# Kernel tuning notes

Measured on AMD Instinct MI355X. Metric: run time of the kernel, lower is better.

Reference implementation:

```python
import jax, jax.numpy as jnp
import numpy as np

CURV_BOUNDS = (-2.0, 2.0)
THRESH = 0.01   # |k| below this -> Euclidean branch
EPS = 1e-5

B, S, D = 4, 2048, 512


def setup_inputs() -> dict:
    key = jax.random.key(0)
    ks = jax.random.split(key, 8)
    x = jax.random.normal(ks[0], (B, S, D), jnp.float32)
    sc = 1.0 / np.sqrt(D)  # ~ nn.Linear default init scale
    Wq = jax.random.uniform(ks[1], (D, D), jnp.float32, -sc, sc)
    bq = jax.random.uniform(ks[2], (D,), jnp.float32, -sc, sc)
    Wk = jax.random.uniform(ks[3], (D, D), jnp.float32, -sc, sc)
    bk = jax.random.uniform(ks[4], (D,), jnp.float32, -sc, sc)
    Wv = jax.random.uniform(ks[5], (D, D), jnp.float32, -sc, sc)
    bv = jax.random.uniform(ks[6], (D,), jnp.float32, -sc, sc)
    curvature_raw = jnp.float32(0.5)   # init_curvature
    temperature = jnp.float32(1.0)
    mask = jnp.triu(jnp.ones((S, S), dtype=bool), 1)  # causal: True = masked out
    return {"x": x, "Wq": Wq, "bq": bq, "Wk": Wk, "bk": bk, "Wv": Wv,
            "bv": bv, "curvature_raw": curvature_raw,
            "temperature": temperature, "mask": mask}


def _curvature(raw):
    k_min, k_max = CURV_BOUNDS
    return k_min + (k_max - k_min) * (jnp.tanh(raw) + 1.0) / 2.0


def _project(u, k):
    # project_to_manifold: identity (euclid), Poincare-ball clip (k<0), sphere renorm (k>0)
    n = jnp.sqrt(jnp.sum(u * u, axis=-1, keepdims=True) + 1e-12)
    absk = jnp.abs(k)
    sk = jnp.sqrt(jnp.maximum(absk, EPS))
    max_norm = (1.0 - 1e-3) / sk                      # ball radius 1/sqrt(|k|)
    u_hyp = u * jnp.minimum(1.0, max_norm / n)
    u_sph = u / (n * sk)                              # sphere radius 1/sqrt(k)
    return jnp.where(absk < THRESH, u, jnp.where(k < 0, u_hyp, u_sph))


def reference(x, Wq, bq, Wk, bk, Wv, bv, curvature_raw, temperature, mask):
    k = _curvature(curvature_raw)
    q = x @ Wq.T + bq
    kk = x @ Wk.T + bk
    v = x @ Wv.T + bv
    qm = _project(q, k)
    km = _project(kk, k)

    # pairwise quantities without materializing [B,S,S,D]
    dots = jnp.einsum('bid,bjd->bij', qm, km)         # [B,S,S]
    qn2 = jnp.sum(qm * qm, axis=-1)                   # [B,S]
    kn2 = jnp.sum(km * km, axis=-1)                   # [B,S]
    diff2 = jnp.maximum(qn2[:, :, None] + kn2[:, None, :] - 2.0 * dots, 0.0)

    absk = jnp.abs(k)
    sk = jnp.sqrt(jnp.maximum(absk, EPS))

    d_euc = jnp.sqrt(diff2 + 1e-12)
    # hyperbolic (Poincare ball, c=|k|): acosh(1 + 2c|x-y|^2 / ((1-c|x|^2)(1-c|y|^2))) / sqrt(c)
    denom = jnp.maximum((1.0 - absk * qn2)[:, :, None] * (1.0 - absk * kn2)[:, None, :], EPS)
    arg = 1.0 + 2.0 * absk * diff2 / denom
    d_hyp = jnp.arccosh(jnp.maximum(arg, 1.0 + 1e-7)) / sk
    # spherical (radius 1/sqrt(k)): arccos(k * <x,y>) / sqrt(k)
    cosang = jnp.clip(absk * dots, -1.0 + 1e-7, 1.0 - 1e-7)
    d_sph = jnp.arccos(cosang) / sk

    dist = jnp.where(absk < THRESH, d_euc, jnp.where(k < 0, d_hyp, d_sph))

    scores = -dist / (temperature + 1e-8)
    scores = jnp.where(mask[None, :, :], -jnp.inf, scores)
    attention = jax.nn.softmax(scores, axis=-1)       # [B,S,S]
    output = jnp.einsum('bij,bjd->bid', attention, v) # [B,S,D]
    return output, attention
```

## Files before the change

### kernel.cpp

```cpp
#include <hip/hip_runtime.h>
#include <hip/hip_bf16.h>
#include <math.h>

typedef unsigned short u16;
typedef float float4e __attribute__((ext_vector_type(4)));
typedef short short8 __attribute__((ext_vector_type(8)));
typedef unsigned short ushort8 __attribute__((ext_vector_type(8)));
typedef unsigned short u16x4 __attribute__((ext_vector_type(4)));

#define SEQ 2048
#define DIM 512
#define NB  4

__device__ __forceinline__ float bf2f(u16 h) {
    return __uint_as_float(((unsigned)h) << 16);
}
__device__ __forceinline__ u16 f2bf(float f) {
    __hip_bfloat16 h = __float2bfloat16(f);
    return *reinterpret_cast<u16*>(&h);
}
__device__ __forceinline__ float curv_of(float raw) {
    return -2.0f + 2.0f * (tanhf(raw) + 1.0f);
}
__device__ __forceinline__ float fast_acos(float x) {
    float ax = fabsf(x);
    float r = sqrtf(fmaxf(1.f - ax, 0.f)) *
              (1.5707288f + ax * (-0.2121144f + ax * (0.0742610f - 0.0187293f * ax)));
    return (x < 0.f) ? (3.14159265f - r) : r;
}
__device__ __forceinline__ void gl_lds16(const u16* g, u16* lds) {
    __builtin_amdgcn_global_load_lds(
        (const __attribute__((address_space(1))) unsigned int*)g,
        (__attribute__((address_space(3))) unsigned int*)lds, 16, 0, 0);
}

__global__ __launch_bounds__(256, 8) void qkv_kernel(
    const float* __restrict__ xf,
    const float* __restrict__ Wq, const float* __restrict__ Wk, const float* __restrict__ Wv,
    const float* __restrict__ bq, const float* __restrict__ bk, const float* __restrict__ bv,
    u16* __restrict__ qk, u16* __restrict__ vT)
{
    int bn = blockIdx.x, bm = blockIdx.y;

    __shared__ __align__(16) u16 As[64 * 64];
    __shared__ __align__(16) u16 Bs[64 * 64];

    int t = threadIdx.x, wave = t >> 6, lane = t & 63;
    int wr = wave >> 1, wc = wave & 1;
    int lrow = lane & 15, quad = lane >> 4;
    int srow = lane >> 3, sc = lane & 7;

    const float* Af = xf + (size_t)(bm * 64) * 512;
    const float* Wsel = (bn < 8) ? Wq : (bn < 16 ? Wk : Wv);
    const float* Bf = Wsel + (size_t)((bn & 7) * 64) * 512;

    float4e acc[2][2];
#pragma unroll
    for (int i = 0; i < 2; i++)
#pragma unroll
        for (int j = 0; j < 2; j++) acc[i][j] = (float4e){0.f, 0.f, 0.f, 0.f};

    for (int kt = 0; kt < 8; ++kt) {
        int k0 = kt << 6;
        __syncthreads();
#pragma unroll
        for (int h = 0; h < 2; ++h) {
            int q = wave * 2 + h;
            int row = q * 8 + srow;
            int c = sc ^ srow;
            const float* ga = Af + (size_t)row * 512 + k0 + c * 8;
            float4 a0 = *(const float4*)ga, a1 = *(const float4*)(ga + 4);
            const float* gb = Bf + (size_t)row * 512 + k0 + c * 8;
            float4 b0 = *(const float4*)gb, b1 = *(const float4*)(gb + 4);
            ushort8 ha, hb;
            ha[0] = f2bf(a0.x); ha[1] = f2bf(a0.y); ha[2] = f2bf(a0.z); ha[3] = f2bf(a0.w);
            ha[4] = f2bf(a1.x); ha[5] = f2bf(a1.y); ha[6] = f2bf(a1.z); ha[7] = f2bf(a1.w);
            hb[0] = f2bf(b0.x); hb[1] = f2bf(b0.y); hb[2] = f2bf(b0.z); hb[3] = f2bf(b0.w);
            hb[4] = f2bf(b1.x); hb[5] = f2bf(b1.y); hb[6] = f2bf(b1.z); hb[7] = f2bf(b1.w);
            *(ushort8*)&As[(size_t)row * 64 + sc * 8] = ha;
            *(ushort8*)&Bs[(size_t)row * 64 + sc * 8] = hb;
        }
        __syncthreads();
#pragma unroll
        for (int s = 0; s < 2; ++s) {
            short8 af[2], bfr[2];
#pragma unroll
            for (int im = 0; im < 2; im++) {
                int R = wr * 32 + im * 16 + lrow;
                af[im] = *(const short8*)&As[R * 64 + (((s * 4 + quad) ^ (R & 7)) * 8)];
            }
#pragma unroll
            for (int in = 0; in < 2; in++) {
                int R = wc * 32 + in * 16 + lrow;
                bfr[in] = *(const short8*)&Bs[R * 64 + (((s * 4 + quad) ^ (R & 7)) * 8)];
            }
#pragma unroll
            for (int im = 0; im < 2; im++)
#pragma unroll
                for (int in = 0; in < 2; in++)
                    acc[im][in] = __builtin_amdgcn_mfma_f32_16x16x32_bf16(af[im], bfr[in], acc[im][in], 0, 0, 0);
        }
    }

#pragma unroll
    for (int im = 0; im < 2; im++)
#pragma unroll
        for (int in = 0; in < 2; in++) {
            int gi0 = bm * 64 + wr * 32 + im * 16 + quad * 4;
            int gj = bn * 64 + wc * 32 + in * 16 + lrow;
            float bias = (gj < 512) ? bq[gj] : (gj < 1024 ? bk[gj - 512] : bv[gj - 1024]);
            if (gj < 1024) {
#pragma unroll
                for (int r = 0; r < 4; r++)
                    qk[(size_t)(gi0 + r) * 1024 + gj] = f2bf(acc[im][in][r] + bias);
            } else {
                u16x4 pack;
#pragma unroll
                for (int r = 0; r < 4; r++) pack[r] = f2bf(acc[im][in][r] + bias);
                int bb = gi0 >> 11, s = gi0 & 2047;
                *(u16x4*)&vT[((size_t)bb * DIM + (gj - 1024)) * SEQ + s] = pack;
            }
        }
}

template<int MODE>
__global__ __launch_bounds__(256, 8) void gemm64_kernel(
    const u16* __restrict__ A, int lda, long long sA,
    const u16* __restrict__ Bt, int ldb, long long sB,
    void* __restrict__ Cv, int ldc, long long sC,
    float* __restrict__ lsum,
    const float* __restrict__ qn2v, const float* __restrict__ kn2v,
    const float* __restrict__ sclqv, const float* __restrict__ sclkv,
    const float* __restrict__ curvp, const float* __restrict__ tempp)
{
    int bn = blockIdx.x, b = blockIdx.z;
    int bm = (MODE == 2) ? (gridDim.y - 1 - blockIdx.y) : blockIdx.y;
    if (MODE == 1 && bn > bm) return;

    __shared__ __align__(16) u16 As[64 * 64];
    __shared__ __align__(16) u16 Bs[64 * 64];

    int t = threadIdx.x, wave = t >> 6, lane = t & 63;
    int wr = wave >> 1, wc = wave & 1;
    int lrow = lane & 15, quad = lane >> 4;
    int srow = lane >> 3, sc = lane & 7;

    const u16* Ab = A + (size_t)b * sA + (size_t)(bm * 64) * lda;
    const u16* Bb = Bt + (size_t)b * sB + (size_t)(bn * 64) * ldb;

    float4e acc[2][2];
#pragma unroll
    for (int i = 0; i < 2; i++)
#pragma unroll
        for (int j = 0; j < 2; j++) acc[i][j] = (float4e){0.f, 0.f, 0.f, 0.f};

    int kIters = (MODE == 2) ? (bm + 1) : 8;

    for (int kt = 0; kt < kIters; ++kt) {
        int k0 = kt << 6;
        __syncthreads();
#pragma unroll
        for (int h = 0; h < 2; ++h) {
            int q = wave * 2 + h;
            int row = q * 8 + srow;
            int c = sc ^ srow;
            gl_lds16(Ab + (size_t)row * lda + k0 + c * 8, &As[q * 512]);
            gl_lds16(Bb + (size_t)row * ldb + k0 + c * 8, &Bs[q * 512]);
        }
        __syncthreads();
#pragma unroll
        for (int s = 0; s < 2; ++s) {
            short8 af[2], bfr[2];
#pragma unroll
            for (int im = 0; im < 2; im++) {
                int R = wr * 32 + im * 16 + lrow;
                af[im] = *(const short8*)&As[R * 64 + (((s * 4 + quad) ^ (R & 7)) * 8)];
            }
#pragma unroll
            for (int in = 0; in < 2; in++) {
                int R = wc * 32 + in * 16 + lrow;
                bfr[in] = *(const short8*)&Bs[R * 64 + (((s * 4 + quad) ^ (R & 7)) * 8)];
            }
#pragma unroll
            for (int im = 0; im < 2; im++)
#pragma unroll
                for (int in = 0; in < 2; in++)
                    acc[im][in] = __builtin_amdgcn_mfma_f32_16x16x32_bf16(af[im], bfr[in], acc[im][in], 0, 0, 0);
        }
    }

    if (MODE == 1) {
        float kv = curv_of(curvp[0]);
        float absk = fabsf(kv);
        float sk = sqrtf(fmaxf(absk, 1e-5f));
        float invsk = 1.0f / sk;
        float invT = 1.0f / (tempp[0] + 1e-8f);
        u16* Cb = (u16*)Cv + (size_t)b * sC;

        float psum[2][4];
#pragma unroll
        for (int im = 0; im < 2; im++)
#pragma unroll
            for (int r = 0; r < 4; r++) psum[im][r] = 0.f;

#pragma unroll
        for (int im = 0; im < 2; im++) {
#pragma unroll
            for (int r = 0; r < 4; r++) {
                int gi = bm * 64 + wr * 32 + im * 16 + quad * 4 + r;
                float qn = qn2v[b * SEQ + gi];
                float sq = sclqv[b * SEQ + gi];
#pragma unroll
                for (int in = 0; in < 2; in++) {
                    int gj = bn * 64 + wc * 32 + in * 16 + lrow;
                    float kn = kn2v[b * SEQ + gj];
                    float dot = acc[im][in][r] * sq * sclkv[b * SEQ + gj];
                    float diff2 = fmaxf(qn + kn - 2.f * dot, 0.f);
                    float dist;
                    if (absk < 0.01f) {
                        dist = sqrtf(diff2 + 1e-12f);
                    } else if (kv < 0.f) {
                        float denom = fmaxf((1.f - absk * qn) * (1.f - absk * kn), 1e-5f);
                        float arg = fmaxf(1.f + 2.f * absk * diff2 / denom, 1.f + 1e-7f);
                        dist = acoshf(arg) * invsk;
                    } else {
                        float c = fminf(fmaxf(absk * dot, -1.f + 1e-7f), 1.f - 1e-7f);
                        dist = fast_acos(c) * invsk;
                    }
                    float s = -dist * invT;
                    float e = (gj <= gi) ? __expf(s) : 0.f;
                    Cb[(size_t)gi * ldc + gj] = f2bf(e);
                    psum[im][r] += e;
                }
            }
        }
#pragma unroll
        for (int im = 0; im < 2; im++)
#pragma unroll
            for (int r = 0; r < 4; r++) {
                float v = psum[im][r];
                v += __shfl_xor(v, 1);
                v += __shfl_xor(v, 2);
                v += __shfl_xor(v, 4);
                v += __shfl_xor(v, 8);
                if (lrow == 0) {
                    int gi = bm * 64 + wr * 32 + im * 16 + quad * 4 + r;
                    atomicAdd(&lsum[b * SEQ + gi], v);
                }
            }
    } else {
        float* Cb = (float*)Cv + (size_t)b * sC;
#pragma unroll
        for (int im = 0; im < 2; im++)
#pragma unroll
            for (int r = 0; r < 4; r++) {
                int gi = bm * 64 + wr * 32 + im * 16 + quad * 4 + r;
                float invl = 1.0f / lsum[b * SEQ + gi];
#pragma unroll
                for (int in = 0; in < 2; in++) {
                    int gd = bn * 64 + wc * 32 + in * 16 + lrow;
                    Cb[(size_t)gi * ldc + gd] = acc[im][in][r] * invl;
                }
            }
    }
}

__global__ __launch_bounds__(256) void project_kernel(
    const u16* __restrict__ qk,
    float* __restrict__ qn2, float* __restrict__ kn2,
    float* __restrict__ sclqv, float* __restrict__ sclkv,
    float* __restrict__ lsum,
    const float* __restrict__ curvp)
{
    if (threadIdx.x < 4) lsum[blockIdx.x * 4 + threadIdx.x] = 0.f;

    int wave = threadIdx.x >> 6, lane = threadIdx.x & 63;
    int r = blockIdx.x * 4 + wave;
    float kv = curv_of(curvp[0]);
    float absk = fabsf(kv);
    float sk = sqrtf(fmaxf(absk, 1e-5f));

    const u16* row = qk + (size_t)r * 1024;
    ushort8 qh = *(const ushort8*)&row[lane * 8];
    ushort8 kh = *(const ushort8*)&row[512 + lane * 8];

    float sq = 0.f, s2 = 0.f;
#pragma unroll
    for (int e = 0; e < 8; e++) {
        float qv = bf2f(qh[e]); sq += qv * qv;
        float kw = bf2f(kh[e]); s2 += kw * kw;
    }
#pragma unroll
    for (int off = 1; off < 64; off <<= 1) {
        sq += __shfl_xor(sq, off);
        s2 += __shfl_xor(s2, off);
    }

    if (lane == 0) {
        float nq = sqrtf(sq + 1e-12f);
        float nk = sqrtf(s2 + 1e-12f);
        float sclq, sclk;
        if (absk < 0.01f) { sclq = 1.f; sclk = 1.f; }
        else if (kv < 0.f) {
            float mx = (1.0f - 1e-3f) / sk;
            sclq = fminf(1.f, mx / nq);
            sclk = fminf(1.f, mx / nk);
        } else {
            sclq = 1.f / (nq * sk);
            sclk = 1.f / (nk * sk);
        }
        qn2[r] = sq * sclq * sclq;
        kn2[r] = s2 * sclk * sclk;
        sclqv[r] = sclq;
        sclkv[r] = sclk;
    }
}

__global__ __launch_bounds__(256) void norm_attn_kernel(
    const u16* __restrict__ attnH, const float* __restrict__ lsum,
    float* __restrict__ attnF)
{
    int i = blockIdx.x, b = blockIdx.y, t = threadIdx.x;
    float inv = 1.0f / lsum[b * SEQ + i];
    const u16* rowh = attnH + ((size_t)b * SEQ + i) * SEQ;
    float* row = attnF + ((size_t)b * SEQ + i) * SEQ;
    int L = i + 1;
    int j0 = t * 8;
    float4 lo, hi;
    if (j0 + 8 <= L) {
        ushort8 h = *(const ushort8*)&rowh[j0];
        lo.x = bf2f(h[0]) * inv; lo.y = bf2f(h[1]) * inv;
        lo.z = bf2f(h[2]) * inv; lo.w = bf2f(h[3]) * inv;
        hi.x = bf2f(h[4]) * inv; hi.y = bf2f(h[5]) * inv;
        hi.z = bf2f(h[6]) * inv; hi.w = bf2f(h[7]) * inv;
    } else {
        float v[8];
#pragma unroll
        for (int e = 0; e < 8; e++)
            v[e] = (j0 + e < L) ? bf2f(rowh[j0 + e]) * inv : 0.f;
        lo = (float4){v[0], v[1], v[2], v[3]};
        hi = (float4){v[4], v[5], v[6], v[7]};
    }
    *(float4*)&row[j0] = lo;
    *(float4*)&row[j0 + 4] = hi;
}

extern "C" void kernel_launch(void* const* d_in, const int* in_sizes, int n_in,
                              void* d_out, int out_size, void* d_ws, size_t ws_size,
                              hipStream_t stream) {
    (void)in_sizes; (void)n_in; (void)out_size; (void)ws_size;

    const float* x    = (const float*)d_in[0];
    const float* Wq   = (const float*)d_in[1];
    const float* bq   = (const float*)d_in[2];
    const float* Wk   = (const float*)d_in[3];
    const float* bk   = (const float*)d_in[4];
    const float* Wv   = (const float*)d_in[5];
    const float* bv   = (const float*)d_in[6];
    const float* curv = (const float*)d_in[7];
    const float* temp = (const float*)d_in[8];

    float* out   = (float*)d_out;
    float* attnF = out + (size_t)NB * SEQ * DIM;

    char* ws = (char*)d_ws;
    u16*   attnH = (u16*)(ws + 0);
    u16*   qk    = (u16*)(ws + 33554432);
    u16*   vT    = (u16*)(ws + 50331648);
    float* qn2   = (float*)(ws + 58720256);
    float* kn2   = (float*)(ws + 58753024);
    float* sclq  = (float*)(ws + 58785792);
    float* sclk  = (float*)(ws + 58818560);
    float* lsum  = (float*)(ws + 58851328);

    qkv_kernel<<<dim3(1536 / 64, 8192 / 64, 1), 256, 0, stream>>>(
        x, Wq, Wk, Wv, bq, bk, bv, qk, vT);

    project_kernel<<<NB * SEQ / 4, 256, 0, stream>>>(qk, qn2, kn2, sclq, sclk, lsum, curv);

    gemm64_kernel<1><<<dim3(SEQ / 64, SEQ / 64, NB), 256, 0, stream>>>(
        qk, 1024, (long long)SEQ * 1024, qk + 512, 1024, (long long)SEQ * 1024,
        (void*)attnH, SEQ, (long long)SEQ * SEQ,
        lsum, qn2, kn2, sclq, sclk, curv, temp);

    gemm64_kernel<2><<<dim3(DIM / 64, SEQ / 64, NB), 256, 0, stream>>>(
        attnH, SEQ, (long long)SEQ * SEQ, vT, SEQ, (long long)DIM * SEQ,
        (void*)out, DIM, (long long)SEQ * DIM,
        lsum, nullptr, nullptr, nullptr, nullptr, nullptr, nullptr);

    norm_attn_kernel<<<dim3(SEQ, NB), 256, 0, stream>>>(attnH, lsum, attnF);
}
```

Measured before the change: 247.1 us.

## Merge PV GEMM and attention normalization into one launch; swizzle QKV block order

The PV GEMM and the attention-row normalization now run as two roles of one kernel. Blocks with x<8 do the PV product and the rest write the normalized fp32 attention tiles, so the bandwidth-bound normalize work overlaps the compute-bound, triangular-imbalanced GEMM instead of running after it. The QKV projection kernel also remaps block ids so groups of 8 row tiles sweep all column tiles together, which is meant to improve L2 reuse of the weights. The cost is that both roles share one launch config and LDS allocation, and the normalize role now uses 64-row tiles.

After: 247.5 us. Within noise of the previous version (+0.2%).

```diff
diff --git a/kernel.cpp b/kernel.cpp
--- a/kernel.cpp
+++ b/kernel.cpp
@@ -40,7 +40,12 @@
     const float* __restrict__ bq, const float* __restrict__ bk, const float* __restrict__ bv,
     u16* __restrict__ qk, u16* __restrict__ vT)
 {
-    int bn = blockIdx.x, bm = blockIdx.y;
+    int id = blockIdx.y * 24 + blockIdx.x;
+    int k8 = id & 7;
+    int rest = id >> 3;
+    int bn = rest % 24;
+    int g  = rest / 24;
+    int bm = g * 8 + k8;
 
     __shared__ __align__(16) u16 As[64 * 64];
     __shared__ __align__(16) u16 Bs[64 * 64];
@@ -123,19 +128,16 @@
         }
 }
 
-template<int MODE>
-__global__ __launch_bounds__(256, 8) void gemm64_kernel(
-    const u16* __restrict__ A, int lda, long long sA,
-    const u16* __restrict__ Bt, int ldb, long long sB,
-    void* __restrict__ Cv, int ldc, long long sC,
+__global__ __launch_bounds__(256, 8) void scores_kernel(
+    const u16* __restrict__ qk,
+    u16* __restrict__ attnH,
     float* __restrict__ lsum,
     const float* __restrict__ qn2v, const float* __restrict__ kn2v,
     const float* __restrict__ sclqv, const float* __restrict__ sclkv,
     const float* __restrict__ curvp, const float* __restrict__ tempp)
 {
-    int bn = blockIdx.x, b = blockIdx.z;
-    int bm = (MODE == 2) ? (gridDim.y - 1 - blockIdx.y) : blockIdx.y;
-    if (MODE == 1 && bn > bm) return;
+    int bn = blockIdx.x, bm = blockIdx.y, b = blockIdx.z;
+    if (bn > bm) return;
 
     __shared__ __align__(16) u16 As[64 * 64];
     __shared__ __align__(16) u16 Bs[64 * 64];
@@ -145,8 +147,8 @@
     int lrow = lane & 15, quad = lane >> 4;
     int srow = lane >> 3, sc = lane & 7;
 
-    const u16* Ab = A + (size_t)b * sA + (size_t)(bm * 64) * lda;
-    const u16* Bb = Bt + (size_t)b * sB + (size_t)(bn * 64) * ldb;
+    const u16* Ab = qk + (size_t)b * SEQ * 1024 + (size_t)(bm * 64) * 1024;
+    const u16* Bb = qk + 512 + (size_t)b * SEQ * 1024 + (size_t)(bn * 64) * 1024;
 
     float4e acc[2][2];
 #pragma unroll
@@ -154,9 +156,7 @@
 #pragma unroll
         for (int j = 0; j < 2; j++) acc[i][j] = (float4e){0.f, 0.f, 0.f, 0.f};
 
-    int kIters = (MODE == 2) ? (bm + 1) : 8;
-
-    for (int kt = 0; kt < kIters; ++kt) {
+    for (int kt = 0; kt < 8; ++kt) {
         int k0 = kt << 6;
         __syncthreads();
 #pragma unroll
@@ -164,8 +164,8 @@
             int q = wave * 2 + h;
             int row = q * 8 + srow;
             int c = sc ^ srow;
-            gl_lds16(Ab + (size_t)row * lda + k0 + c * 8, &As[q * 512]);
-            gl_lds16(Bb + (size_t)row * ldb + k0 + c * 8, &Bs[q * 512]);
+            gl_lds16(Ab + (size_t)row * 1024 + k0 + c * 8, &As[q * 512]);
+            gl_lds16(Bb + (size_t)row * 1024 + k0 + c * 8, &Bs[q * 512]);
         }
         __syncthreads();
 #pragma unroll
@@ -189,67 +189,129 @@
         }
     }
 
-    if (MODE == 1) {
-        float kv = curv_of(curvp[0]);
-        float absk = fabsf(kv);
-        float sk = sqrtf(fmaxf(absk, 1e-5f));
-        float invsk = 1.0f / sk;
-        float invT = 1.0f / (tempp[0] + 1e-8f);
-        u16* Cb = (u16*)Cv + (size_t)b * sC;
-
-        float psum[2][4];
-#pragma unroll
-        for (int im = 0; im < 2; im++)
-#pragma unroll
-            for (int r = 0; r < 4; r++) psum[im][r] = 0.f;
-
-#pragma unroll
-        for (int im = 0; im < 2; im++) {
-#pragma unroll
-            for (int r = 0; r < 4; r++) {
+    float kv = curv_of(curvp[0]);
+    float absk = fabsf(kv);
+    float sk = sqrtf(fmaxf(absk, 1e-5f));
+    float invsk = 1.0f / sk;
+    float invT = 1.0f / (tempp[0] + 1e-8f);
+    u16* Cb = attnH + (size_t)b * SEQ * SEQ;
+
+    float psum[2][4];
+#pragma unroll
+    for (int im = 0; im < 2; im++)
+#pragma unroll
+        for (int r = 0; r < 4; r++) psum[im][r] = 0.f;
+
+#pragma unroll
+    for (int im = 0; im < 2; im++) {
+#pragma unroll
+        for (int r = 0; r < 4; r++) {
+            int gi = bm * 64 + wr * 32 + im * 16 + quad * 4 + r;
+            float qn = qn2v[b * SEQ + gi];
+            float sq = sclqv[b * SEQ + gi];
+#pragma unroll
+            for (int in = 0; in < 2; in++) {
+                int gj = bn * 64 + wc * 32 + in * 16 + lrow;
+                float kn = kn2v[b * SEQ + gj];
+                float dot = acc[im][in][r] * sq * sclkv[b * SEQ + gj];
+                float diff2 = fmaxf(qn + kn - 2.f * dot, 0.f);
+                float dist;
+                if (absk < 0.01f) {
+                    dist = sqrtf(diff2 + 1e-12f);
+                } else if (kv < 0.f) {
+                    float denom = fmaxf((1.f - absk * qn) * (1.f - absk * kn), 1e-5f);
+                    float arg = fmaxf(1.f + 2.f * absk * diff2 / denom, 1.f + 1e-7f);
+                    dist = acoshf(arg) * invsk;
+                } else {
+                    float c = fminf(fmaxf(absk * dot, -1.f + 1e-7f), 1.f - 1e-7f);
+                    dist = fast_acos(c) * invsk;
+                }
+                float s = -dist * invT;
+                float e = (gj <= gi) ? __expf(s) : 0.f;
+                Cb[(size_t)gi * SEQ + gj] = f2bf(e);
+                psum[im][r] += e;
+            }
+        }
+    }
+#pragma unroll
+    for (int im = 0; im < 2; im++)
+#pragma unroll
+        for (int r = 0; r < 4; r++) {
+            float v = psum[im][r];
+            v += __shfl_xor(v, 1);
+            v += __shfl_xor(v, 2);
+            v += __shfl_xor(v, 4);
+            v += __shfl_xor(v, 8);
+            if (lrow == 0) {
                 int gi = bm * 64 + wr * 32 + im * 16 + quad * 4 + r;
-                float qn = qn2v[b * SEQ + gi];
-                float sq = sclqv[b * SEQ + gi];
+                atomicAdd(&lsum[b * SEQ + gi], v);
+            }
+        }
+}
+
+__global__ __launch_bounds__(256, 8) void pv_norm_kernel(
+    const u16* __restrict__ attnH, const u16* __restrict__ vT,
+    const float* __restrict__ lsum,
+    float* __restrict__ out, float* __restrict__ attnF)
+{
+    __shared__ __align__(16) u16 As[64 * 64];
+    __shared__ __align__(16) u16 Bs[64 * 64];
+
+    int b = blockIdx.z;
+    int t = threadIdx.x;
+
+    if (blockIdx.x < 8) {
+        int bn = blockIdx.x;
+        int bm = 31 - blockIdx.y;
+        int wave = t >> 6, lane = t & 63;
+        int wr = wave >> 1, wc = wave & 1;
+        int lrow = lane & 15, quad = lane >> 4;
+        int srow = lane >> 3, sc = lane & 7;
+
+        const u16* Ab = attnH + (size_t)b * SEQ * SEQ + (size_t)(bm * 64) * SEQ;
+        const u16* Bb = vT + (size_t)b * DIM * SEQ + (size_t)(bn * 64) * SEQ;
+
+        float4e acc[2][2];
+#pragma unroll
+        for (int i = 0; i < 2; i++)
+#pragma unroll
+            for (int j = 0; j < 2; j++) acc[i][j] = (float4e){0.f, 0.f, 0.f, 0.f};
+
+        int kIters = bm + 1;
+        for (int kt = 0; kt < kIters; ++kt) {
+            int k0 = kt << 6;
+            __syncthreads();
+#pragma unroll
+            for (int h = 0; h < 2; ++h) {
+                int q = wave * 2 + h;
+                int row = q * 8 + srow;
+                int c = sc ^ srow;
+                gl_lds16(Ab + (size_t)row * SEQ + k0 + c * 8, &As[q * 512]);
+                gl_lds16(Bb + (size_t)row * SEQ + k0 + c * 8, &Bs[q * 512]);
+            }
+            __syncthreads();
+#pragma unroll
+            for (int s = 0; s < 2; ++s) {
+                short8 af[2], bfr[2];
+#pragma unroll
+                for (int im = 0; im < 2; im++) {
+                    int R = wr * 32 + im * 16 + lrow;
+                    af[im] = *(const short8*)&As[R * 64 + (((s * 4 + quad) ^ (R & 7)) * 8)];
+                }
 #pragma unroll
                 for (int in = 0; in < 2; in++) {
-                    int gj = bn * 64 + wc * 32 + in * 16 + lrow;
-                    float kn = kn2v[b * SEQ + gj];
-                    float dot = acc[im][in][r] * sq * sclkv[b * SEQ + gj];
-                    float diff2 = fmaxf(qn + kn - 2.f * dot, 0.f);
-                    float dist;
-                    if (absk < 0.01f) {
-                        dist = sqrtf(diff2 + 1e-12f);
-                    } else if (kv < 0.f) {
-                        float denom = fmaxf((1.f - absk * qn) * (1.f - absk * kn), 1e-5f);
-                        float arg = fmaxf(1.f + 2.f * absk * diff2 / denom, 1.f + 1e-7f);
-                        dist = acoshf(arg) * invsk;
-                    } else {
-                        float c = fminf(fmaxf(absk * dot, -1.f + 1e-7f), 1.f - 1e-7f);
-                        dist = fast_acos(c) * invsk;
-                    }
-                    float s = -dist * invT;
-                    float e = (gj <= gi) ? __expf(s) : 0.f;
-                    Cb[(size_t)gi * ldc + gj] = f2bf(e);
-                    psum[im][r] += e;
+                    int R = wc * 32 + in * 16 + lrow;
+                    bfr[in] = *(const short8*)&Bs[R * 64 + (((s * 4 + quad) ^ (R & 7)) * 8)];
                 }
-            }
-        }
-#pragma unroll
-        for (int im = 0; im < 2; im++)
-#pragma unroll
-            for (int r = 0; r < 4; r++) {
-                float v = psum[im][r];
-                v += __shfl_xor(v, 1);
-                v += __shfl_xor(v, 2);
-                v += __shfl_xor(v, 4);
-                v += __shfl_xor(v, 8);
-                if (lrow == 0) {
-                    int gi = bm * 64 + wr * 32 + im * 16 + quad * 4 + r;
-                    atomicAdd(&lsum[b * SEQ + gi], v);
-                }
-            }
-    } else {
-        float* Cb = (float*)Cv + (size_t)b * sC;
+#pragma unroll
+                for (int im = 0; im < 2; im++)
+#pragma unroll
+                    for (int in = 0; in < 2; in++)
+                        acc[im][in] = __builtin_amdgcn_mfma_f32_16x16x32_bf16(af[im], bfr[in], acc[im][in], 0, 0, 0);
+            }
+        }
+
+        float* Cb = out + (size_t)b * SEQ * DIM;
 #pragma unroll
         for (int im = 0; im < 2; im++)
 #pragma unroll
@@ -259,9 +321,32 @@
 #pragma unroll
                 for (int in = 0; in < 2; in++) {
                     int gd = bn * 64 + wc * 32 + in * 16 + lrow;
-                    Cb[(size_t)gi * ldc + gd] = acc[im][in][r] * invl;
+                    Cb[(size_t)gi * DIM + gd] = acc[im][in][r] * invl;
                 }
             }
+    } else {
+        int s = blockIdx.x - 8;
+        int by = blockIdx.y;
+        int cq = t & 63, rr4 = t >> 6;
+        const u16* Ab = attnH + (size_t)b * SEQ * SEQ;
+        float* Fb = attnF + (size_t)b * SEQ * SEQ;
+        int j = s * 256 + cq * 4;
+#pragma unroll
+        for (int p = 0; p < 16; ++p) {
+            int i = by * 64 + p * 4 + rr4;
+            float4 v;
+            if (j > i) {
+                v = (float4){0.f, 0.f, 0.f, 0.f};
+            } else {
+                float inv = 1.0f / lsum[b * SEQ + i];
+                u16x4 h = *(const u16x4*)&Ab[(size_t)i * SEQ + j];
+                v.x = bf2f(h[0]) * inv;
+                v.y = (j + 1 <= i) ? bf2f(h[1]) * inv : 0.f;
+                v.z = (j + 2 <= i) ? bf2f(h[2]) * inv : 0.f;
+                v.w = (j + 3 <= i) ? bf2f(h[3]) * inv : 0.f;
+            }
+            *(float4*)&Fb[(size_t)i * SEQ + j] = v;
+        }
     }
 }
 
@@ -316,35 +401,6 @@
     }
 }
 
-__global__ __launch_bounds__(256) void norm_attn_kernel(
-    const u16* __restrict__ attnH, const float* __restrict__ lsum,
-    float* __restrict__ attnF)
-{
-    int i = blockIdx.x, b = blockIdx.y, t = threadIdx.x;
-    float inv = 1.0f / lsum[b * SEQ + i];
-    const u16* rowh = attnH + ((size_t)b * SEQ + i) * SEQ;
-    float* row = attnF + ((size_t)b * SEQ + i) * SEQ;
-    int L = i + 1;
-    int j0 = t * 8;
-    float4 lo, hi;
-    if (j0 + 8 <= L) {
-        ushort8 h = *(const ushort8*)&rowh[j0];
-        lo.x = bf2f(h[0]) * inv; lo.y = bf2f(h[1]) * inv;
-        lo.z = bf2f(h[2]) * inv; lo.w = bf2f(h[3]) * inv;
-        hi.x = bf2f(h[4]) * inv; hi.y = bf2f(h[5]) * inv;
-        hi.z = bf2f(h[6]) * inv; hi.w = bf2f(h[7]) * inv;
-    } else {
-        float v[8];
-#pragma unroll
-        for (int e = 0; e < 8; e++)
-            v[e] = (j0 + e < L) ? bf2f(rowh[j0 + e]) * inv : 0.f;
-        lo = (float4){v[0], v[1], v[2], v[3]};
-        hi = (float4){v[4], v[5], v[6], v[7]};
-    }
-    *(float4*)&row[j0] = lo;
-    *(float4*)&row[j0 + 4] = hi;
-}
-
 extern "C" void kernel_launch(void* const* d_in, const int* in_sizes, int n_in,
                               void* d_out, int out_size, void* d_ws, size_t ws_size,
                               hipStream_t stream) {
@@ -373,20 +429,14 @@
     float* sclk  = (float*)(ws + 58818560);
     float* lsum  = (float*)(ws + 58851328);
 
-    qkv_kernel<<<dim3(1536 / 64, 8192 / 64, 1), 256, 0, stream>>>(
+    qkv_kernel<<<dim3(24, 128, 1), 256, 0, stream>>>(
         x, Wq, Wk, Wv, bq, bk, bv, qk, vT);
 
     project_kernel<<<NB * SEQ / 4, 256, 0, stream>>>(qk, qn2, kn2, sclq, sclk, lsum, curv);
 
-    gemm64_kernel<1><<<dim3(SEQ / 64, SEQ / 64, NB), 256, 0, stream>>>(
-        qk, 1024, (long long)SEQ * 1024, qk + 512, 1024, (long long)SEQ * 1024,
-        (void*)attnH, SEQ, (long long)SEQ * SEQ,
-        lsum, qn2, kn2, sclq, sclk, curv, temp);
-
-    gemm64_kernel<2><<<dim3(DIM / 64, SEQ / 64, NB), 256, 0, stream>>>(
-        attnH, SEQ, (long long)SEQ * SEQ, vT, SEQ, (long long)DIM * SEQ,
-        (void*)out, DIM, (long long)SEQ * DIM,
-        lsum, nullptr, nullptr, nullptr, nullptr, nullptr, nullptr);
-
-    norm_attn_kernel<<<dim3(SEQ, NB), 256, 0, stream>>>(attnH, lsum, attnF);
-}
+    scores_kernel<<<dim3(SEQ / 64, SEQ / 64, NB), 256, 0, stream>>>(
+        qk, attnH, lsum, qn2, kn2, sclq, sclk, curv, temp);
+
+    pv_norm_kernel<<<dim3(16, 32, NB), 256, 0, stream>>>(
+        attnH, vT, lsum, out, attnF);
+}
```
